# Kernel optimization log

Hardware: AMD Instinct MI355X
Metric: run time of the kernel (lower is better)

The kernel has to match this reference:

```python
import jax, jax.numpy as jnp
import numpy as np

K = 3      # kernel size
S = 1      # stride
P = 1      # padding
D = 1      # dilation
KK = K * K


def _conv2d(x, w, b):
    y = jax.lax.conv_general_dilated(
        x, w, window_strides=(S, S), padding=[(P, P), (P, P)],
        rhs_dilation=(D, D), dimension_numbers=('NCHW', 'OIHW', 'NCHW'))
    return y + b[None, :, None, None]


def _bilinear_gather(x, py, px):
    # x: [B,C,H,W]; py,px: [B,KK,Ho,Wo] absolute (possibly out-of-bounds) coords
    B, C, H, W = x.shape
    y0 = jnp.floor(py)
    x0 = jnp.floor(px)
    wy1 = py - y0
    wx1 = px - x0
    wy0 = 1.0 - wy1
    wx0 = 1.0 - wx1

    def gather(yi, xi):
        valid = (yi >= 0) & (yi <= H - 1) & (xi >= 0) & (xi <= W - 1)
        yc = jnp.clip(yi, 0, H - 1).astype(jnp.int32)
        xc = jnp.clip(xi, 0, W - 1).astype(jnp.int32)
        # per-batch fancy gather -> [B,C,KK,Ho,Wo]
        g = jax.vmap(lambda xb, yb, xb_i: xb[:, yb, xb_i])(x, yc, xc)
        return g * valid[:, None].astype(x.dtype)

    v = (gather(y0, x0) * (wy0 * wx0)[:, None]
         + gather(y0, x0 + 1) * (wy0 * wx1)[:, None]
         + gather(y0 + 1, x0) * (wy1 * wx0)[:, None]
         + gather(y0 + 1, x0 + 1) * (wy1 * wx1)[:, None])
    return v  # [B,C,KK,Ho,Wo]


def _dcnv2(x, weight, bias, offset_w, offset_b):
    B, C, H, W = x.shape
    om = _conv2d(x, offset_w, offset_b)              # [B, 3*KK, Ho, Wo]
    offset = om[:, :2 * KK]
    mask = jax.nn.sigmoid(om[:, 2 * KK:])            # [B, KK, Ho, Wo]
    Ho, Wo = om.shape[2], om.shape[3]
    off = offset.reshape(B, KK, 2, Ho, Wo)           # (dy, dx) per kernel tap
    dy, dx = off[:, :, 0], off[:, :, 1]
    ki, kj = jnp.meshgrid(jnp.arange(K), jnp.arange(K), indexing='ij')
    # base sampling grid for each output pixel and kernel tap
    base_y = (jnp.arange(Ho) * S - P)[None, :] + (ki.reshape(KK) * D)[:, None]  # [KK,Ho]
    base_x = (jnp.arange(Wo) * S - P)[None, :] + (kj.reshape(KK) * D)[:, None]  # [KK,Wo]
    py = dy + base_y[None, :, :, None].astype(dy.dtype)   # [B,KK,Ho,Wo]
    px = dx + base_x[None, :, None, :].astype(dx.dtype)   # [B,KK,Ho,Wo]
    sampled = _bilinear_gather(x, py, px) * mask[:, None]  # [B,C,KK,Ho,Wo]
    out = jnp.einsum('bckhw,ock->bohw', sampled,
                     weight.reshape(weight.shape[0], C, KK))
    return out + bias[None, :, None, None]


def setup_inputs() -> dict:
    key = jax.random.key(0)
    k1, k2, k3, k4 = jax.random.split(key, 4)
    B, Cin, Cout, H, W = 8, 256, 256, 64, 64
    stdv = 1.0 / np.sqrt(Cin * K * K)
    x = jax.random.normal(k1, (B, Cin, H, W), dtype=jnp.float32)
    weight = jax.random.normal(k2, (Cout, Cin, K, K), dtype=jnp.float32) * stdv
    bias = jax.random.normal(k3, (Cout,), dtype=jnp.float32) * 0.01
    # small offset-conv weights so learned offsets stay a few pixels
    offset_w = jax.random.normal(k4, (3 * KK, Cin, K, K), dtype=jnp.float32) * 0.01
    offset_b = jnp.zeros((3 * KK,), dtype=jnp.float32)
    return {"x": x, "weight": weight, "bias": bias,
            "offset_w": offset_w, "offset_b": offset_b}


def reference(x, weight, bias, offset_w, offset_b):
    return _dcnv2(x, weight, bias, offset_w, offset_b)
```

## Files before the change

### kernel.cpp

```cpp
#include <hip/hip_runtime.h>
#include <math.h>

#define CIN 256
#define HH 64
#define WW 64
#define BB 8
#define HW 4096
#define KDIM 2304
#define NPIX9 (BB*9*HH*WW)

typedef __attribute__((ext_vector_type(8))) short bf16x8;
typedef __attribute__((ext_vector_type(4))) float f32x4;

__device__ __forceinline__ unsigned short f2bf(float f) {
    unsigned int u = __float_as_uint(f);
    u += 0x7fffu + ((u >> 16) & 1u);
    return (unsigned short)(u >> 16);
}

#define GLDS16(gp, lp) __builtin_amdgcn_global_load_lds( \
    (const __attribute__((address_space(1))) unsigned int*)(gp), \
    (__attribute__((address_space(3))) unsigned int*)(lp), 16, 0, 0)

__global__ __launch_bounds__(256) void pack_bsw(const float* __restrict__ weight,
                                                unsigned short* __restrict__ Bsw) {
    int oc = blockIdx.x;
    int c  = threadIdx.x;
    int cc = c >> 6, kc = c & 63;
    int swz = (oc & 7) << 3;
    const float* wp = weight + (size_t)oc * KDIM + c * 9;
    #pragma unroll
    for (int tap = 0; tap < 9; ++tap) {
        Bsw[(size_t)oc * KDIM + tap * 256 + cc * 64 + (kc ^ swz)] = f2bf(wp[tap]);
    }
}

__global__ __launch_bounds__(256) void pack_b2(const float* __restrict__ ow,
                                               unsigned short* __restrict__ B2sw) {
    int oc = blockIdx.x;
    int c  = threadIdx.x;
    int swz = (oc & 7) << 3;
    #pragma unroll
    for (int tap = 0; tap < 9; ++tap) {
        int k = c * 9 + tap;
        int pos = (k & ~63) | ((k & 63) ^ swz);
        unsigned short v = 0;
        if (oc < 27) v = f2bf(ow[(size_t)oc * KDIM + k]);
        B2sw[(size_t)oc * KDIM + pos] = v;
    }
}

__global__ __launch_bounds__(256) void offset_gemm(
    const float* __restrict__ x, const unsigned short* __restrict__ B2sw,
    const float* __restrict__ ob,
    int* __restrict__ off00, int* __restrict__ off01,
    int* __restrict__ off10, int* __restrict__ off11,
    float* __restrict__ ww00, float* __restrict__ ww01,
    float* __restrict__ ww10, float* __restrict__ ww11)
{
    __shared__ unsigned short A_lds[64][64];
    __shared__ unsigned short B2_lds[32][64];
    __shared__ float om[64][33];

    const int blk = blockIdx.x;
    const int b = blk >> 6, h = blk & 63;
    const int t = threadIdx.x;
    const int p = t & 63;
    const int wv = t >> 6;
    const int ln = t & 63;

    f32x4 acc[2];
    #pragma unroll
    for (int n = 0; n < 2; ++n) acc[n] = (f32x4){0.f, 0.f, 0.f, 0.f};

    const float* xb = x + (size_t)b * CIN * HW;
    const int swzp = (p & 7) << 3;

    for (int ch = 0; ch < 36; ++ch) {
        const int k0 = ch * 64;
        __syncthreads();
        {
            const unsigned short* gp = B2sw + (size_t)(wv * 8 + (ln >> 3)) * KDIM
                                     + k0 + (ln & 7) * 8;
            GLDS16(gp, &B2_lds[wv * 8][0]);
        }
        #pragma unroll
        for (int g = 0; g < 2; ++g) {
            bf16x8 pk;
            #pragma unroll
            for (int i = 0; i < 8; ++i) {
                int k = k0 + wv * 16 + g * 8 + i;
                int c = (k * 7282) >> 16;
                int tp = k - c * 9;
                int ki = (tp * 11) >> 5;
                int kj = tp - ki * 3;
                int yy = h - 1 + ki;
                int xx = p - 1 + kj;
                bool ok = ((unsigned)yy < 64u) && ((unsigned)xx < 64u);
                float v = ok ? xb[(size_t)c * HW + yy * WW + xx] : 0.f;
                pk[i] = (short)f2bf(v);
            }
            *(bf16x8*)&A_lds[p][(wv * 16 + g * 8) ^ swzp] = pk;
        }
        __syncthreads();
        #pragma unroll
        for (int ks = 0; ks < 2; ++ks) {
            const int kg = ks * 32 + ((ln >> 4) << 3);
            const int arow = wv * 16 + (ln & 15);
            bf16x8 af = *(const bf16x8*)&A_lds[arow][kg ^ ((arow & 7) << 3)];
            #pragma unroll
            for (int n = 0; n < 2; ++n) {
                const int brow = n * 16 + (ln & 15);
                bf16x8 bf = *(const bf16x8*)&B2_lds[brow][kg ^ ((brow & 7) << 3)];
                acc[n] = __builtin_amdgcn_mfma_f32_16x16x32_bf16(af, bf, acc[n], 0, 0, 0);
            }
        }
    }

    __syncthreads();
    #pragma unroll
    for (int n = 0; n < 2; ++n)
        #pragma unroll
        for (int r = 0; r < 4; ++r)
            om[wv * 16 + ((ln >> 4) << 2) + r][n * 16 + (ln & 15)] = acc[n][r];
    __syncthreads();

    for (int rep = 0; rep < 3; ++rep) {
        int idx = rep * 256 + t;
        if (idx < 576) {
            int k = idx >> 6, w2 = idx & 63;
            float dy = om[w2][2 * k]     + ob[2 * k];
            float dx = om[w2][2 * k + 1] + ob[2 * k + 1];
            float mv = om[w2][18 + k]    + ob[18 + k];
            float m = 1.f / (1.f + expf(-mv));

            float py = dy + (float)(h - 1 + k / 3);
            float px = dx + (float)(w2 - 1 + k % 3);
            float y0f = floorf(py), x0f = floorf(px);
            float wy1 = py - y0f, wx1 = px - x0f;
            float wy0 = 1.f - wy1, wx0 = 1.f - wx1;
            int iy0 = (int)y0f, ix0 = (int)x0f;
            int iy1 = iy0 + 1, ix1 = ix0 + 1;
            bool vy0 = (iy0 >= 0) & (iy0 < HH);
            bool vy1 = (iy1 >= 0) & (iy1 < HH);
            bool vx0 = (ix0 >= 0) & (ix0 < WW);
            bool vx1 = (ix1 >= 0) & (ix1 < WW);
            int cy0 = min(max(iy0, 0), HH - 1), cy1 = min(max(iy1, 0), HH - 1);
            int cx0 = min(max(ix0, 0), WW - 1), cx1 = min(max(ix1, 0), WW - 1);
            size_t ridx = ((size_t)(b * 9 + k) * HH + h) * WW + w2;
            off00[ridx] = cy0 * WW + cx0;
            off01[ridx] = cy0 * WW + cx1;
            off10[ridx] = cy1 * WW + cx0;
            off11[ridx] = cy1 * WW + cx1;
            ww00[ridx] = (vy0 && vx0) ? wy0 * wx0 * m : 0.f;
            ww01[ridx] = (vy0 && vx1) ? wy0 * wx1 * m : 0.f;
            ww10[ridx] = (vy1 && vx0) ? wy1 * wx0 * m : 0.f;
            ww11[ridx] = (vy1 && vx1) ? wy1 * wx1 * m : 0.f;
        }
    }
}

__global__ __launch_bounds__(256, 2) void main_gemm(
    const float* __restrict__ x, const unsigned short* __restrict__ Bsw,
    const float* __restrict__ bias,
    const int* __restrict__ off00, const int* __restrict__ off01,
    const int* __restrict__ off10, const int* __restrict__ off11,
    const float* __restrict__ ww00, const float* __restrict__ ww01,
    const float* __restrict__ ww10, const float* __restrict__ ww11,
    float* __restrict__ out)
{
    __shared__ unsigned short A_lds[64][64];
    __shared__ unsigned short B_lds[256][64];

    const int blk = blockIdx.x;
    const int b = blk >> 6, h = blk & 63;
    const int t = threadIdx.x;
    const int p = t & 63;
    const int wv = t >> 6;
    const int ln = t & 63;

    f32x4 acc[4][4];
    #pragma unroll
    for (int m = 0; m < 4; ++m)
        #pragma unroll
        for (int n = 0; n < 4; ++n) acc[m][n] = (f32x4){0.f, 0.f, 0.f, 0.f};

    const float* xb = x + (size_t)b * CIN * HW;
    const int swzp = (p & 7) << 3;

    for (int tap = 0; tap < 9; ++tap) {
        const size_t ridx = ((size_t)(b * 9 + tap) * HH + h) * WW + p;
        const int o00 = off00[ridx], o01 = off01[ridx];
        const int o10 = off10[ridx], o11 = off11[ridx];
        const float f00 = ww00[ridx], f01 = ww01[ridx];
        const float f10 = ww10[ridx], f11 = ww11[ridx];

        for (int cc = 0; cc < 4; ++cc) {
            __syncthreads();
            {
                const unsigned short* gbase = Bsw + (size_t)(ln >> 3) * KDIM
                                            + tap * 256 + cc * 64 + (ln & 7) * 8;
                #pragma unroll
                for (int it = 0; it < 8; ++it) {
                    const int r0 = wv * 64 + it * 8;
                    GLDS16(gbase + (size_t)r0 * KDIM, &B_lds[r0][0]);
                }
            }
            {
                const float* xs = xb + (size_t)(cc * 64 + wv * 16) * HW;
                #pragma unroll
                for (int g = 0; g < 2; ++g) {
                    bf16x8 pk;
                    #pragma unroll
                    for (int i = 0; i < 8; ++i) {
                        float v = f00 * xs[o00] + f01 * xs[o01]
                                + f10 * xs[o10] + f11 * xs[o11];
                        pk[i] = (short)f2bf(v);
                        xs += HW;
                    }
                    *(bf16x8*)&A_lds[p][(wv * 16 + g * 8) ^ swzp] = pk;
                }
            }
            __syncthreads();
            #pragma unroll
            for (int ks = 0; ks < 2; ++ks) {
                const int kg = ks * 32 + ((ln >> 4) << 3);
                bf16x8 af[4], bfr[4];
                #pragma unroll
                for (int m = 0; m < 4; ++m) {
                    const int row = m * 16 + (ln & 15);
                    af[m] = *(const bf16x8*)&A_lds[row][kg ^ ((row & 7) << 3)];
                }
                #pragma unroll
                for (int n = 0; n < 4; ++n) {
                    const int row = wv * 64 + n * 16 + (ln & 15);
                    bfr[n] = *(const bf16x8*)&B_lds[row][kg ^ ((row & 7) << 3)];
                }
                #pragma unroll
                for (int m = 0; m < 4; ++m)
                    #pragma unroll
                    for (int n = 0; n < 4; ++n)
                        acc[m][n] = __builtin_amdgcn_mfma_f32_16x16x32_bf16(
                            af[m], bfr[n], acc[m][n], 0, 0, 0);
            }
        }
    }

    #pragma unroll
    for (int n = 0; n < 4; ++n) {
        const int oc = wv * 64 + n * 16 + (ln & 15);
        const float bs = bias[oc];
        float* orow = out + ((size_t)(b * 256 + oc) * HH + h) * WW;
        #pragma unroll
        for (int m = 0; m < 4; ++m) {
            f32x4 v = acc[m][n];
            float4 s;
            s.x = v[0] + bs; s.y = v[1] + bs; s.z = v[2] + bs; s.w = v[3] + bs;
            *(float4*)&orow[m * 16 + ((ln >> 4) << 2)] = s;
        }
    }
}

extern "C" void kernel_launch(void* const* d_in, const int* in_sizes, int n_in,
                              void* d_out, int out_size, void* d_ws, size_t ws_size,
                              hipStream_t stream) {
    const float* x        = (const float*)d_in[0];
    const float* weight   = (const float*)d_in[1];
    const float* bias     = (const float*)d_in[2];
    const float* offset_w = (const float*)d_in[3];
    const float* offset_b = (const float*)d_in[4];
    float* out = (float*)d_out;
    float* ws  = (float*)d_ws;

    unsigned short* Bsw  = (unsigned short*)ws;
    unsigned short* B2sw = (unsigned short*)(ws + 294912);
    float* rec = ws + 294912 + 36864;
    int*   off00 = (int*)(rec + 0 * (size_t)NPIX9);
    int*   off01 = (int*)(rec + 1 * (size_t)NPIX9);
    int*   off10 = (int*)(rec + 2 * (size_t)NPIX9);
    int*   off11 = (int*)(rec + 3 * (size_t)NPIX9);
    float* ww00  = rec + 4 * (size_t)NPIX9;
    float* ww01  = rec + 5 * (size_t)NPIX9;
    float* ww10  = rec + 6 * (size_t)NPIX9;
    float* ww11  = rec + 7 * (size_t)NPIX9;

    pack_bsw<<<256, 256, 0, stream>>>(weight, Bsw);
    pack_b2<<<32, 256, 0, stream>>>(offset_w, B2sw);
    offset_gemm<<<BB * HH, 256, 0, stream>>>(x, B2sw, offset_b,
                                             off00, off01, off10, off11,
                                             ww00, ww01, ww10, ww11);
    main_gemm<<<BB * HH, 256, 0, stream>>>(x, Bsw, bias,
                                           off00, off01, off10, off11,
                                           ww00, ww01, ww10, ww11, out);
}
```

Before: 424.5 us.

## Double-buffer LDS and prefetch next K-chunk in offset and main GEMMs

Both GEMM kernels now use 512-thread blocks covering two output rows (128 pixels), with double-buffered A and B tiles in LDS. The next chunk's global gathers and weight loads are issued before the current chunk's MFMAs, so memory latency overlaps with compute and only one barrier is needed per chunk. The offset weights are repacked in tap-major order so each K-chunk maps to a single tap and channel block, which removes the per-element div/mod index math. In exchange, register and LDS pressure rise (launch bounds 512,1), the grid shrinks to 256 blocks, and that may lower occupancy on a chip with many CUs.

```diff
diff --git a/kernel.cpp b/kernel.cpp
--- a/kernel.cpp
+++ b/kernel.cpp
@@ -39,18 +39,17 @@
                                                unsigned short* __restrict__ B2sw) {
     int oc = blockIdx.x;
     int c  = threadIdx.x;
+    int cc = c >> 6, kc = c & 63;
     int swz = (oc & 7) << 3;
     #pragma unroll
     for (int tap = 0; tap < 9; ++tap) {
-        int k = c * 9 + tap;
-        int pos = (k & ~63) | ((k & 63) ^ swz);
         unsigned short v = 0;
-        if (oc < 27) v = f2bf(ow[(size_t)oc * KDIM + k]);
-        B2sw[(size_t)oc * KDIM + pos] = v;
-    }
-}
-
-__global__ __launch_bounds__(256) void offset_gemm(
+        if (oc < 27) v = f2bf(ow[(size_t)oc * KDIM + c * 9 + tap]);
+        B2sw[(size_t)oc * KDIM + tap * 256 + cc * 64 + (kc ^ swz)] = v;
+    }
+}
+
+__global__ __launch_bounds__(512, 1) void offset_gemm(
     const float* __restrict__ x, const unsigned short* __restrict__ B2sw,
     const float* __restrict__ ob,
     int* __restrict__ off00, int* __restrict__ off01,
@@ -58,66 +57,95 @@
     float* __restrict__ ww00, float* __restrict__ ww01,
     float* __restrict__ ww10, float* __restrict__ ww11)
 {
-    __shared__ unsigned short A_lds[64][64];
-    __shared__ unsigned short B2_lds[32][64];
-    __shared__ float om[64][33];
-
-    const int blk = blockIdx.x;
-    const int b = blk >> 6, h = blk & 63;
+    __shared__ unsigned short A_lds[2][128][64];
+    __shared__ unsigned short B2_lds[2][32][64];
+    __shared__ float om[128][33];
+
+    const int mb = blockIdx.x;
+    const int b = mb & 7;
+    const int h0 = (mb >> 3) * 2;
     const int t = threadIdx.x;
-    const int p = t & 63;
-    const int wv = t >> 6;
-    const int ln = t & 63;
+    const int wv = t >> 6, ln = t & 63;
+    const int p = t & 127;
+    const int oct0 = t >> 7;
+    const int hP = h0 + (p >> 6), wP = p & 63;
+    const int swzp = (p & 7) << 3;
 
     f32x4 acc[2];
-    #pragma unroll
-    for (int n = 0; n < 2; ++n) acc[n] = (f32x4){0.f, 0.f, 0.f, 0.f};
+    acc[0] = (f32x4){0.f,0.f,0.f,0.f};
+    acc[1] = (f32x4){0.f,0.f,0.f,0.f};
 
     const float* xb = x + (size_t)b * CIN * HW;
-    const int swzp = (p & 7) << 3;
-
-    for (int ch = 0; ch < 36; ++ch) {
-        const int k0 = ch * 64;
-        __syncthreads();
-        {
+
+    {
+        if (wv < 4) {
             const unsigned short* gp = B2sw + (size_t)(wv * 8 + (ln >> 3)) * KDIM
-                                     + k0 + (ln & 7) * 8;
-            GLDS16(gp, &B2_lds[wv * 8][0]);
-        }
+                                     + (ln & 7) * 8;
+            GLDS16(gp, &B2_lds[0][wv * 8][0]);
+        }
+        int y = hP - 1, xx = wP - 1;
+        bool ok = ((unsigned)y < 64u) & ((unsigned)xx < 64u);
+        const float* bp = xb + (y * WW + xx);
         #pragma unroll
         for (int g = 0; g < 2; ++g) {
+            const int k8 = oct0 * 8 + g * 32;
             bf16x8 pk;
             #pragma unroll
             for (int i = 0; i < 8; ++i) {
-                int k = k0 + wv * 16 + g * 8 + i;
-                int c = (k * 7282) >> 16;
-                int tp = k - c * 9;
-                int ki = (tp * 11) >> 5;
-                int kj = tp - ki * 3;
-                int yy = h - 1 + ki;
-                int xx = p - 1 + kj;
-                bool ok = ((unsigned)yy < 64u) && ((unsigned)xx < 64u);
-                float v = ok ? xb[(size_t)c * HW + yy * WW + xx] : 0.f;
+                float v = ok ? bp[(size_t)(k8 + i) * HW] : 0.f;
                 pk[i] = (short)f2bf(v);
             }
-            *(bf16x8*)&A_lds[p][(wv * 16 + g * 8) ^ swzp] = pk;
-        }
-        __syncthreads();
+            *(bf16x8*)&A_lds[0][p][k8 ^ swzp] = pk;
+        }
+    }
+    __syncthreads();
+
+    for (int kk = 0; kk < 36; ++kk) {
+        const int cur = kk & 1;
+        const bool pre = kk < 35;
+        float xr[16];
+        if (pre) {
+            const int kn = kk + 1, tapn = kn >> 2, ccn = kn & 3;
+            if (wv < 4) {
+                const unsigned short* gp = B2sw + (size_t)(wv * 8 + (ln >> 3)) * KDIM
+                                         + tapn * 256 + ccn * 64 + (ln & 7) * 8;
+                GLDS16(gp, &B2_lds[cur ^ 1][wv * 8][0]);
+            }
+            const int ki = (tapn * 11) >> 5, kj = tapn - ki * 3;
+            int y = hP - 1 + ki, xx = wP - 1 + kj;
+            bool ok = ((unsigned)y < 64u) & ((unsigned)xx < 64u);
+            const float* bp = xb + (size_t)(ccn * 64) * HW + (y * WW + xx);
+            #pragma unroll
+            for (int g = 0; g < 2; ++g)
+                #pragma unroll
+                for (int i = 0; i < 8; ++i)
+                    xr[g * 8 + i] = ok ? bp[(size_t)(oct0 * 8 + g * 32 + i) * HW] : 0.f;
+        }
         #pragma unroll
         for (int ks = 0; ks < 2; ++ks) {
             const int kg = ks * 32 + ((ln >> 4) << 3);
-            const int arow = wv * 16 + (ln & 15);
-            bf16x8 af = *(const bf16x8*)&A_lds[arow][kg ^ ((arow & 7) << 3)];
+            const int ar = wv * 16 + (ln & 15);
+            bf16x8 af = *(const bf16x8*)&A_lds[cur][ar][kg ^ ((ar & 7) << 3)];
             #pragma unroll
             for (int n = 0; n < 2; ++n) {
-                const int brow = n * 16 + (ln & 15);
-                bf16x8 bf = *(const bf16x8*)&B2_lds[brow][kg ^ ((brow & 7) << 3)];
-                acc[n] = __builtin_amdgcn_mfma_f32_16x16x32_bf16(af, bf, acc[n], 0, 0, 0);
-            }
-        }
-    }
-
-    __syncthreads();
+                const int br = n * 16 + (ln & 15);
+                bf16x8 bfr = *(const bf16x8*)&B2_lds[cur][br][kg ^ ((br & 7) << 3)];
+                acc[n] = __builtin_amdgcn_mfma_f32_16x16x32_bf16(af, bfr, acc[n], 0, 0, 0);
+            }
+        }
+        if (pre) {
+            #pragma unroll
+            for (int g = 0; g < 2; ++g) {
+                const int k8 = oct0 * 8 + g * 32;
+                bf16x8 pk;
+                #pragma unroll
+                for (int i = 0; i < 8; ++i) pk[i] = (short)f2bf(xr[g * 8 + i]);
+                *(bf16x8*)&A_lds[cur ^ 1][p][k8 ^ swzp] = pk;
+            }
+        }
+        __syncthreads();
+    }
+
     #pragma unroll
     for (int n = 0; n < 2; ++n)
         #pragma unroll
@@ -125,13 +153,15 @@
             om[wv * 16 + ((ln >> 4) << 2) + r][n * 16 + (ln & 15)] = acc[n][r];
     __syncthreads();
 
+    #pragma unroll
     for (int rep = 0; rep < 3; ++rep) {
-        int idx = rep * 256 + t;
-        if (idx < 576) {
-            int k = idx >> 6, w2 = idx & 63;
-            float dy = om[w2][2 * k]     + ob[2 * k];
-            float dx = om[w2][2 * k + 1] + ob[2 * k + 1];
-            float mv = om[w2][18 + k]    + ob[18 + k];
+        int idx = rep * 512 + t;
+        if (idx < 1152) {
+            int k = idx >> 7, p2 = idx & 127;
+            int h = h0 + (p2 >> 6), w2 = p2 & 63;
+            float dy = om[p2][2 * k]     + ob[2 * k];
+            float dx = om[p2][2 * k + 1] + ob[2 * k + 1];
+            float mv = om[p2][18 + k]    + ob[18 + k];
             float m = 1.f / (1.f + expf(-mv));
 
             float py = dy + (float)(h - 1 + k / 3);
@@ -160,7 +190,7 @@
     }
 }
 
-__global__ __launch_bounds__(256, 2) void main_gemm(
+__global__ __launch_bounds__(512, 1) void main_gemm(
     const float* __restrict__ x, const unsigned short* __restrict__ Bsw,
     const float* __restrict__ bias,
     const int* __restrict__ off00, const int* __restrict__ off01,
@@ -169,94 +199,167 @@
     const float* __restrict__ ww10, const float* __restrict__ ww11,
     float* __restrict__ out)
 {
-    __shared__ unsigned short A_lds[64][64];
-    __shared__ unsigned short B_lds[256][64];
-
-    const int blk = blockIdx.x;
-    const int b = blk >> 6, h = blk & 63;
+    __shared__ unsigned short A_lds[2][128][64];
+    __shared__ unsigned short B_lds[2][256][64];
+
+    const int mb = blockIdx.x;
+    const int b = mb & 7;
+    const int h0 = (mb >> 3) * 2;
     const int t = threadIdx.x;
-    const int p = t & 63;
-    const int wv = t >> 6;
-    const int ln = t & 63;
+    const int wv = t >> 6, ln = t & 63;
+    const int wm = wv >> 2, wn = wv & 3;
+    const int p = t & 127;
+    const int oct0 = t >> 7;
+    const int hP = h0 + (p >> 6), wP = p & 63;
+    const int swzp = (p & 7) << 3;
 
     f32x4 acc[4][4];
     #pragma unroll
     for (int m = 0; m < 4; ++m)
         #pragma unroll
-        for (int n = 0; n < 4; ++n) acc[m][n] = (f32x4){0.f, 0.f, 0.f, 0.f};
+        for (int n = 0; n < 4; ++n) acc[m][n] = (f32x4){0.f,0.f,0.f,0.f};
 
     const float* xb = x + (size_t)b * CIN * HW;
-    const int swzp = (p & 7) << 3;
-
-    for (int tap = 0; tap < 9; ++tap) {
-        const size_t ridx = ((size_t)(b * 9 + tap) * HH + h) * WW + p;
+
+    {
+        const unsigned short* gb = Bsw + (size_t)(ln >> 3) * KDIM + (ln & 7) * 8;
+        #pragma unroll
+        for (int it = 0; it < 4; ++it) {
+            const int r0 = wv * 32 + it * 8;
+            GLDS16(gb + (size_t)r0 * KDIM, &B_lds[0][r0][0]);
+        }
+        const size_t ridx = ((size_t)(b * 9) * HH + hP) * WW + wP;
         const int o00 = off00[ridx], o01 = off01[ridx];
         const int o10 = off10[ridx], o11 = off11[ridx];
         const float f00 = ww00[ridx], f01 = ww01[ridx];
         const float f10 = ww10[ridx], f11 = ww11[ridx];
-
-        for (int cc = 0; cc < 4; ++cc) {
-            __syncthreads();
-            {
-                const unsigned short* gbase = Bsw + (size_t)(ln >> 3) * KDIM
-                                            + tap * 256 + cc * 64 + (ln & 7) * 8;
+        #pragma unroll
+        for (int g = 0; g < 2; ++g) {
+            const int k8 = oct0 * 8 + g * 32;
+            bf16x8 pk;
+            #pragma unroll
+            for (int i = 0; i < 8; ++i) {
+                const float* xs = xb + (size_t)(k8 + i) * HW;
+                float v = f00 * xs[o00] + f01 * xs[o01]
+                        + f10 * xs[o10] + f11 * xs[o11];
+                pk[i] = (short)f2bf(v);
+            }
+            *(bf16x8*)&A_lds[0][p][k8 ^ swzp] = pk;
+        }
+    }
+    __syncthreads();
+
+    for (int kk = 0; kk < 36; ++kk) {
+        const int cur = kk & 1;
+        const bool pre = kk < 35;
+        float c00[16], c01[16], c10[16], c11[16];
+        float f00 = 0.f, f01 = 0.f, f10 = 0.f, f11 = 0.f;
+        int o00 = 0, o01 = 0, o10 = 0, o11 = 0;
+        const float* xc = xb;
+        if (pre) {
+            const int kn = kk + 1, tapn = kn >> 2, ccn = kn & 3;
+            const unsigned short* gb = Bsw + (size_t)(ln >> 3) * KDIM
+                                     + tapn * 256 + ccn * 64 + (ln & 7) * 8;
+            #pragma unroll
+            for (int it = 0; it < 4; ++it) {
+                const int r0 = wv * 32 + it * 8;
+                GLDS16(gb + (size_t)r0 * KDIM, &B_lds[cur ^ 1][r0][0]);
+            }
+            const size_t ridx = ((size_t)(b * 9 + tapn) * HH + hP) * WW + wP;
+            o00 = off00[ridx]; o01 = off01[ridx];
+            o10 = off10[ridx]; o11 = off11[ridx];
+            f00 = ww00[ridx]; f01 = ww01[ridx];
+            f10 = ww10[ridx]; f11 = ww11[ridx];
+            xc = xb + (size_t)(ccn * 64 + oct0 * 8) * HW;
+            #pragma unroll
+            for (int i = 0; i < 8; ++i) {
+                const float* xs = xc + (size_t)i * HW;
+                c00[i] = xs[o00]; c01[i] = xs[o01];
+                c10[i] = xs[o10]; c11[i] = xs[o11];
+            }
+        }
+        {
+            const int kg = (ln >> 4) << 3;
+            bf16x8 af[4], bfr[4];
+            #pragma unroll
+            for (int m = 0; m < 4; ++m) {
+                const int row = wm * 64 + m * 16 + (ln & 15);
+                af[m] = *(const bf16x8*)&A_lds[cur][row][kg ^ ((row & 7) << 3)];
+            }
+            #pragma unroll
+            for (int n = 0; n < 4; ++n) {
+                const int row = wn * 64 + n * 16 + (ln & 15);
+                bfr[n] = *(const bf16x8*)&B_lds[cur][row][kg ^ ((row & 7) << 3)];
+            }
+            #pragma unroll
+            for (int m = 0; m < 4; ++m)
                 #pragma unroll
-                for (int it = 0; it < 8; ++it) {
-                    const int r0 = wv * 64 + it * 8;
-                    GLDS16(gbase + (size_t)r0 * KDIM, &B_lds[r0][0]);
-                }
-            }
-            {
-                const float* xs = xb + (size_t)(cc * 64 + wv * 16) * HW;
+                for (int n = 0; n < 4; ++n)
+                    acc[m][n] = __builtin_amdgcn_mfma_f32_16x16x32_bf16(
+                        af[m], bfr[n], acc[m][n], 0, 0, 0);
+        }
+        if (pre) {
+            bf16x8 pk;
+            #pragma unroll
+            for (int i = 0; i < 8; ++i) {
+                float v = f00 * c00[i] + f01 * c01[i]
+                        + f10 * c10[i] + f11 * c11[i];
+                pk[i] = (short)f2bf(v);
+            }
+            *(bf16x8*)&A_lds[cur ^ 1][p][(oct0 * 8) ^ swzp] = pk;
+            const float* xc1 = xc + (size_t)32 * HW;
+            #pragma unroll
+            for (int i = 0; i < 8; ++i) {
+                const float* xs = xc1 + (size_t)i * HW;
+                c00[8 + i] = xs[o00]; c01[8 + i] = xs[o01];
+                c10[8 + i] = xs[o10]; c11[8 + i] = xs[o11];
+            }
+        }
+        {
+            const int kg = 32 + ((ln >> 4) << 3);
+            bf16x8 af[4], bfr[4];
+            #pragma unroll
+            for (int m = 0; m < 4; ++m) {
+                const int row = wm * 64 + m * 16 + (ln & 15);
+                af[m] = *(const bf16x8*)&A_lds[cur][row][kg ^ ((row & 7) << 3)];
+            }
+            #pragma unroll
+            for (int n = 0; n < 4; ++n) {
+                const int row = wn * 64 + n * 16 + (ln & 15);
+                bfr[n] = *(const bf16x8*)&B_lds[cur][row][kg ^ ((row & 7) << 3)];
+            }
+            #pragma unroll
+            for (int m = 0; m < 4; ++m)
                 #pragma unroll
-                for (int g = 0; g < 2; ++g) {
-                    bf16x8 pk;
-                    #pragma unroll
-                    for (int i = 0; i < 8; ++i) {
-                        float v = f00 * xs[o00] + f01 * xs[o01]
-                                + f10 * xs[o10] + f11 * xs[o11];
-                        pk[i] = (short)f2bf(v);
-                        xs += HW;
-                    }
-                    *(bf16x8*)&A_lds[p][(wv * 16 + g * 8) ^ swzp] = pk;
-                }
-            }
-            __syncthreads();
-            #pragma unroll
-            for (int ks = 0; ks < 2; ++ks) {
-                const int kg = ks * 32 + ((ln >> 4) << 3);
-                bf16x8 af[4], bfr[4];
-                #pragma unroll
-                for (int m = 0; m < 4; ++m) {
-                    const int row = m * 16 + (ln & 15);
-                    af[m] = *(const bf16x8*)&A_lds[row][kg ^ ((row & 7) << 3)];
-                }
-                #pragma unroll
-                for (int n = 0; n < 4; ++n) {
-                    const int row = wv * 64 + n * 16 + (ln & 15);
-                    bfr[n] = *(const bf16x8*)&B_lds[row][kg ^ ((row & 7) << 3)];
-                }
-                #pragma unroll
-                for (int m = 0; m < 4; ++m)
-                    #pragma unroll
-                    for (int n = 0; n < 4; ++n)
-                        acc[m][n] = __builtin_amdgcn_mfma_f32_16x16x32_bf16(
-                            af[m], bfr[n], acc[m][n], 0, 0, 0);
-            }
-        }
+                for (int n = 0; n < 4; ++n)
+                    acc[m][n] = __builtin_amdgcn_mfma_f32_16x16x32_bf16(
+                        af[m], bfr[n], acc[m][n], 0, 0, 0);
+        }
+        if (pre) {
+            bf16x8 pk;
+            #pragma unroll
+            for (int i = 0; i < 8; ++i) {
+                float v = f00 * c00[8 + i] + f01 * c01[8 + i]
+                        + f10 * c10[8 + i] + f11 * c11[8 + i];
+                pk[i] = (short)f2bf(v);
+            }
+            *(bf16x8*)&A_lds[cur ^ 1][p][(oct0 * 8 + 32) ^ swzp] = pk;
+        }
+        __syncthreads();
     }
 
     #pragma unroll
     for (int n = 0; n < 4; ++n) {
-        const int oc = wv * 64 + n * 16 + (ln & 15);
+        const int oc = wn * 64 + n * 16 + (ln & 15);
         const float bs = bias[oc];
-        float* orow = out + ((size_t)(b * 256 + oc) * HH + h) * WW;
         #pragma unroll
         for (int m = 0; m < 4; ++m) {
+            const int pix = wm * 64 + m * 16 + ((ln >> 4) << 2);
+            const int h = h0 + (pix >> 6), w0 = pix & 63;
             f32x4 v = acc[m][n];
             float4 s;
             s.x = v[0] + bs; s.y = v[1] + bs; s.z = v[2] + bs; s.w = v[3] + bs;
-            *(float4*)&orow[m * 16 + ((ln >> 4) << 2)] = s;
+            *(float4*)&out[((size_t)(b * 256 + oc) * HH + h) * WW + w0] = s;
         }
     }
 }
@@ -286,10 +389,10 @@
 
     pack_bsw<<<256, 256, 0, stream>>>(weight, Bsw);
     pack_b2<<<32, 256, 0, stream>>>(offset_w, B2sw);
-    offset_gemm<<<BB * HH, 256, 0, stream>>>(x, B2sw, offset_b,
-                                             off00, off01, off10, off11,
-                                             ww00, ww01, ww10, ww11);
-    main_gemm<<<BB * HH, 256, 0, stream>>>(x, Bsw, bias,
-                                           off00, off01, off10, off11,
-                                           ww00, ww01, ww10, ww11, out);
-}
+    offset_gemm<<<256, 512, 0, stream>>>(x, B2sw, offset_b,
+                                         off00, off01, off10, off11,
+                                         ww00, ww01, ww10, ww11);
+    main_gemm<<<256, 512, 0, stream>>>(x, Bsw, bias,
+                                       off00, off01, off10, off11,
+                                       ww00, ww01, ww10, ww11, out);
+}
```

After: 342.4 us. 1.24x faster.
